# Kernel tuning notes

Measured on AMD Instinct MI355X. Metric: run time of the kernel, lower is better.

The kernel has to match this reference:

```python
import jax, jax.numpy as jnp
import numpy as np

D_MODEL, N_HEADS, D_HEAD, D_FF, N_LAYERS, VOCAB = 768, 12, 64, 3072, 4, 32000
B, S = 4, 1024
EPS = 1e-5
NEG = -1000000000.0


def layer_norm(x, gamma, beta):
    mean = jnp.mean(x, axis=-1, keepdims=True)
    var = jnp.mean((x - mean) ** 2, axis=-1, keepdims=True)
    return gamma * ((x - mean) / jnp.sqrt(var + EPS)) + beta


def gelu_lean(x):
    return x * (0.5 * (1.0 + jnp.tanh(0.7978845608 * (x + 0.044715 * x * x * x))))


def positional_encoding(seq_len, dim, dtype):
    idx = jnp.arange(dim)
    exponent = (2 * (idx // 2)).astype(dtype) / float(dim)
    pos = jnp.arange(seq_len, dtype=dtype)[:, None]
    angle = pos / jnp.power(jnp.asarray(10000.0, dtype), exponent[None, :])
    return jnp.where((idx % 2 == 0)[None, :], jnp.sin(angle), jnp.cos(angle))


def setup_inputs() -> dict:
    key = jax.random.key(0)
    ks = jax.random.split(key, 10)
    std = 0.02
    inp = {
        "tokens": jax.random.randint(ks[0], (B, S), 0, VOCAB),
        "predict_idx": 1023,
        "embedding": std * jax.random.normal(ks[1], (D_MODEL, VOCAB), jnp.float32),
        "ln1_g": jnp.ones((N_LAYERS, D_MODEL), jnp.float32),
        "ln1_b": jnp.zeros((N_LAYERS, D_MODEL), jnp.float32),
        "wq": std * jax.random.normal(ks[2], (N_LAYERS, N_HEADS, D_HEAD, D_MODEL), jnp.float32),
        "wk": std * jax.random.normal(ks[3], (N_LAYERS, N_HEADS, D_HEAD, D_MODEL), jnp.float32),
        "wv": std * jax.random.normal(ks[4], (N_LAYERS, N_HEADS, D_HEAD, D_MODEL), jnp.float32),
        "wo": std * jax.random.normal(ks[5], (N_LAYERS, D_MODEL, N_HEADS * D_HEAD), jnp.float32),
        "ln2_g": jnp.ones((N_LAYERS, D_MODEL), jnp.float32),
        "ln2_b": jnp.zeros((N_LAYERS, D_MODEL), jnp.float32),
        "fc1": std * jax.random.normal(ks[6], (N_LAYERS, D_FF, D_MODEL), jnp.float32),
        "fc2": std * jax.random.normal(ks[7], (N_LAYERS, D_MODEL, D_FF), jnp.float32),
        "lnf_g": jnp.ones((D_MODEL,), jnp.float32),
        "lnf_b": jnp.zeros((D_MODEL,), jnp.float32),
        "unembed": std * jax.random.normal(ks[8], (VOCAB, D_MODEL), jnp.float32),
    }
    return inp


def reference(tokens, predict_idx, embedding, ln1_g, ln1_b, wq, wk, wv, wo,
              ln2_g, ln2_b, fc1, fc2, lnf_g, lnf_b, unembed):
    dtype = embedding.dtype
    b, s = tokens.shape
    d_head = wq.shape[2]
    scale = 1.0 / float(np.sqrt(d_head))

    # token embedding [B,S,D] + sinusoidal positions
    x = embedding.T[tokens] + positional_encoding(s, embedding.shape[0], dtype)[None]

    # causal mask: True above the diagonal -> filled with -1e9
    causal = jnp.triu(jnp.ones((s, s), bool), k=1)

    for l in range(wq.shape[0]):
        h = layer_norm(x, ln1_g[l], ln1_b[l])
        q = jnp.einsum('bsd,hed->bhse', h, wq[l])
        k = jnp.einsum('bsd,hed->bhse', h, wk[l])
        v = jnp.einsum('bsd,hed->bhse', h, wv[l])
        scores = jnp.einsum('bhse,bhte->bhst', q, k) * scale
        scores = jnp.where(causal[None, None], NEG, scores)
        weights = jax.nn.softmax(scores, axis=-1)
        attn = jnp.einsum('bhst,bhte->bhse', weights, v)  # [B,H,S,dh]
        attn = attn.transpose(0, 2, 1, 3).reshape(b, s, -1)  # concat heads
        x = x + attn @ wo[l].T
        h2 = layer_norm(x, ln2_g[l], ln2_b[l])
        x = x + gelu_lean(h2 @ fc1[l].T) @ fc2[l].T

    selected = x[:, predict_idx, :]  # [B, D]
    normed = layer_norm(selected, lnf_g, lnf_b)
    return normed @ unembed.T  # [B, vocab]
```

## Files before the change

kernel.cpp:

```cpp
#include <hip/hip_runtime.h>
#include <hip/hip_bf16.h>

#define D_MODEL 768
#define N_HEADS 12
#define D_HEAD  64
#define D_FF    3072
#define N_LAYERS 4
#define VOCAB   32000
#define BATCH   4
#define SEQ     1024
#define NROWS   (BATCH*SEQ)
#define NEGV    -1000000000.0f
#define LN_EPS  1e-5f

typedef __attribute__((ext_vector_type(8))) short bf16x8;
typedef __attribute__((ext_vector_type(4))) float f32x4;
typedef __attribute__((ext_vector_type(8))) unsigned short u16x8;
typedef __attribute__((ext_vector_type(4))) unsigned short u16x4;

typedef __attribute__((address_space(1))) const unsigned int g_u32;
typedef __attribute__((address_space(3))) unsigned int l_u32;

__device__ __forceinline__ float bf2f(unsigned short u) {
  return __uint_as_float(((unsigned int)u) << 16);
}
__device__ __forceinline__ unsigned short f2bf(float f) {
  __hip_bfloat16 h = __float2bfloat16(f);
  return *reinterpret_cast<unsigned short*>(&h);
}

__device__ __forceinline__ float block_reduce_sum(float v, float* sbuf) {
#pragma unroll
  for (int off = 32; off > 0; off >>= 1) v += __shfl_down(v, off, 64);
  int lane = threadIdx.x & 63, wid = threadIdx.x >> 6;
  if (lane == 0) sbuf[wid] = v;
  __syncthreads();
  if (threadIdx.x == 0) sbuf[4] = sbuf[0] + sbuf[1] + sbuf[2] + sbuf[3];
  __syncthreads();
  return sbuf[4];
}

__device__ __forceinline__ float gelu_f(float x) {
  float z2 = 1.5957691216f * x * (1.0f + 0.044715f * x * x);
  return x / (1.0f + __expf(-z2));
}

__global__ __launch_bounds__(256) void qkv_pack_kernel(
    const float* __restrict__ wq, const float* __restrict__ wk,
    const float* __restrict__ wv, __hip_bfloat16* __restrict__ dst)
{
  const int WMAT = D_MODEL * D_MODEL;
  long long i = (long long)(blockIdx.x * 256 + threadIdx.x) * 8;
  long long l = i / (3LL * WMAT);
  long long rem = i - l * 3LL * WMAT;
  int which = (int)(rem / WMAT);
  long long off = rem - (long long)which * WMAT;
  const float* src = (which == 0 ? wq : which == 1 ? wk : wv) + l * WMAT + off;
  float4 a = *(const float4*)src;
  float4 b = *(const float4*)(src + 4);
  struct bf8 { __hip_bfloat16 h[8]; } r;
  r.h[0] = __float2bfloat16(a.x); r.h[1] = __float2bfloat16(a.y);
  r.h[2] = __float2bfloat16(a.z); r.h[3] = __float2bfloat16(a.w);
  r.h[4] = __float2bfloat16(b.x); r.h[5] = __float2bfloat16(b.y);
  r.h[6] = __float2bfloat16(b.z); r.h[7] = __float2bfloat16(b.w);
  *(bf8*)(dst + i) = r;
}

__global__ __launch_bounds__(256) void convert3_kernel(
    const float* __restrict__ wo, const float* __restrict__ fc1,
    const float* __restrict__ fc2, __hip_bfloat16* __restrict__ dst)
{
  const long long WM4 = 4LL * D_MODEL * D_MODEL;
  const long long FM4 = 4LL * D_FF * D_MODEL;
  long long i = (long long)(blockIdx.x * 256 + threadIdx.x) * 8;
  const float* src;
  if (i < WM4)            src = wo  + i;
  else if (i < WM4 + FM4) src = fc1 + (i - WM4);
  else                    src = fc2 + (i - WM4 - FM4);
  float4 a = *(const float4*)src;
  float4 b = *(const float4*)(src + 4);
  struct bf8 { __hip_bfloat16 h[8]; } r;
  r.h[0] = __float2bfloat16(a.x); r.h[1] = __float2bfloat16(a.y);
  r.h[2] = __float2bfloat16(a.z); r.h[3] = __float2bfloat16(a.w);
  r.h[4] = __float2bfloat16(b.x); r.h[5] = __float2bfloat16(b.y);
  r.h[6] = __float2bfloat16(b.z); r.h[7] = __float2bfloat16(b.w);
  *(bf8*)(dst + i) = r;
}

__global__ __launch_bounds__(256) void transpose_emb_kernel(
    const float* __restrict__ emb, __hip_bfloat16* __restrict__ embT)
{
  __shared__ float tile[64][65];
  const int vb = blockIdx.x * 64;
  const int db = blockIdx.y * 64;
  const int tid = threadIdx.x;
  {
    int r = tid >> 4, c = (tid & 15) * 4;
#pragma unroll
    for (int p = 0; p < 4; ++p) {
      float4 v = *(const float4*)(emb + (size_t)(db + r + p * 16) * VOCAB + vb + c);
      tile[c + 0][r + p * 16] = v.x;
      tile[c + 1][r + p * 16] = v.y;
      tile[c + 2][r + p * 16] = v.z;
      tile[c + 3][r + p * 16] = v.w;
    }
  }
  __syncthreads();
  {
    int v = tid >> 2, d0 = (tid & 3) * 16;
    unsigned short* op = (unsigned short*)embT + (size_t)(vb + v) * D_MODEL + db + d0;
    u16x8 o0, o1;
#pragma unroll
    for (int j = 0; j < 8; ++j) {
      o0[j] = f2bf(tile[v][d0 + j]);
      o1[j] = f2bf(tile[v][d0 + 8 + j]);
    }
    *(u16x8*)op = o0;
    *(u16x8*)(op + 8) = o1;
  }
}

__global__ __launch_bounds__(256) void embed_kernel(
    const int* __restrict__ tokens, const __hip_bfloat16* __restrict__ embT,
    float* __restrict__ x)
{
  int bs = blockIdx.x;
  int s = bs & (SEQ - 1);
  int tok = tokens[bs];
  const unsigned short* ep = (const unsigned short*)embT + (size_t)tok * D_MODEL;
  for (int d = threadIdx.x; d < D_MODEL; d += 256) {
    float ev = bf2f(ep[d]);
    int dpair = d & ~1;
    float expo = (float)dpair * (1.0f / (float)D_MODEL);
    float ang = (float)s / powf(10000.0f, expo);
    float pe = (d & 1) ? cosf(ang) : sinf(ang);
    x[(size_t)bs * D_MODEL + d] = ev + pe;
  }
}

__global__ __launch_bounds__(256) void ln_kernel(
    const float* __restrict__ in, __hip_bfloat16* __restrict__ out,
    const float* __restrict__ g, const float* __restrict__ bb)
{
  __shared__ float sbuf[8];
  size_t row = blockIdx.x;
  const float* rp = in + row * D_MODEL;
  int t = threadIdx.x;
  float x0 = rp[t], x1 = rp[t + 256], x2 = rp[t + 512];
  float mean = block_reduce_sum(x0 + x1 + x2, sbuf) * (1.0f / (float)D_MODEL);
  float d0 = x0 - mean, d1 = x1 - mean, d2 = x2 - mean;
  float var = block_reduce_sum(d0*d0 + d1*d1 + d2*d2, sbuf) * (1.0f / (float)D_MODEL);
  float rstd = rsqrtf(var + LN_EPS);
  __hip_bfloat16* op = out + row * D_MODEL;
  op[t]       = __float2bfloat16(g[t]       * (d0 * rstd) + bb[t]);
  op[t + 256] = __float2bfloat16(g[t + 256] * (d1 * rstd) + bb[t + 256]);
  op[t + 512] = __float2bfloat16(g[t + 512] * (d2 * rstd) + bb[t + 512]);
}

__global__ __launch_bounds__(256) void final_ln_kernel(
    const float* __restrict__ x, const int* __restrict__ pidx,
    const float* __restrict__ g, const float* __restrict__ bb,
    float* __restrict__ out)
{
  __shared__ float sbuf[8];
  int p = pidx[0];
  const float* rp = x + ((size_t)blockIdx.x * SEQ + p) * D_MODEL;
  int t = threadIdx.x;
  float x0 = rp[t], x1 = rp[t + 256], x2 = rp[t + 512];
  float mean = block_reduce_sum(x0 + x1 + x2, sbuf) * (1.0f / (float)D_MODEL);
  float d0 = x0 - mean, d1 = x1 - mean, d2 = x2 - mean;
  float var = block_reduce_sum(d0*d0 + d1*d1 + d2*d2, sbuf) * (1.0f / (float)D_MODEL);
  float rstd = rsqrtf(var + LN_EPS);
  float* op = out + (size_t)blockIdx.x * D_MODEL;
  op[t]       = g[t]       * (d0 * rstd) + bb[t];
  op[t + 256] = g[t + 256] * (d1 * rstd) + bb[t + 256];
  op[t + 512] = g[t + 512] * (d2 * rstd) + bb[t + 512];
}

__device__ __forceinline__ int2 xcd_tile(int gx, int gy) {
  int flat = blockIdx.y * gx + blockIdx.x;
  int cpx = (gx * gy) >> 3;
  int logical = (flat & 7) * cpx + (flat >> 3);
  return make_int2(logical % gx, logical / gx);
}

#define WAITV4() asm volatile("s_waitcnt vmcnt(4)" ::: "memory")
#define WAITV0() asm volatile("s_waitcnt vmcnt(0)" ::: "memory")
#define MEMFENCE() asm volatile("" ::: "memory")

__global__ __launch_bounds__(256) void gemm_bf16_kernel(
    const __hip_bfloat16* __restrict__ A, const __hip_bfloat16* __restrict__ W,
    void* __restrict__ Cv, const float* __restrict__ resid,
    int N, int K, int mode)
{
  __shared__ __align__(16) unsigned short As[3][128 * 32];
  __shared__ __align__(16) unsigned short Bs[3][128 * 32];
  const unsigned short* Au = (const unsigned short*)A;
  const unsigned short* Wu = (const unsigned short*)W;
  const int tid = threadIdx.x;
  const int wv = tid >> 6, ln = tid & 63;
  const int l15 = ln & 15, l4 = ln >> 4;
  int2 tc = xcd_tile(N >> 7, gridDim.y);
  const int bm = tc.y * 128, bn = tc.x * 128;
  const int wr = wv >> 1, wc = wv & 1;

  const int lrow = wv * 16 + (ln >> 2);
  const int schunk = (ln & 3) ^ ((ln >> 3) & 3);
  const size_t gA0 = (size_t)(bm + lrow) * K + schunk * 8;
  const size_t gA1 = (size_t)(bm + 64 + lrow) * K + schunk * 8;
  const size_t gB0 = (size_t)(bn + lrow) * K + schunk * 8;
  const size_t gB1 = (size_t)(bn + 64 + lrow) * K + schunk * 8;
  const int ldsb = wv * 512;

#define STAGE128(buf, k0)                                                          \
  {                                                                                \
    __builtin_amdgcn_global_load_lds((g_u32*)(Au + gA0 + (k0)), (l_u32*)(As[buf] + ldsb), 16, 0, 0);        \
    __builtin_amdgcn_global_load_lds((g_u32*)(Au + gA1 + (k0)), (l_u32*)(As[buf] + 2048 + ldsb), 16, 0, 0); \
    __builtin_amdgcn_global_load_lds((g_u32*)(Wu + gB0 + (k0)), (l_u32*)(Bs[buf] + ldsb), 16, 0, 0);        \
    __builtin_amdgcn_global_load_lds((g_u32*)(Wu + gB1 + (k0)), (l_u32*)(Bs[buf] + 2048 + ldsb), 16, 0, 0); \
  }

  const int rslot = (l4 ^ ((l15 >> 1) & 3)) * 8;

#define COMPUTE128(buf)                                                            \
  {                                                                                \
    bf16x8 af[4], bfr[4];                                                          \
    _Pragma("unroll")                                                              \
    for (int m = 0; m < 4; ++m)                                                    \
      af[m] = *(const bf16x8*)(As[buf] + (wr * 64 + m * 16 + l15) * 32 + rslot);   \
    _Pragma("unroll")                                                              \
    for (int n = 0; n < 4; ++n)                                                    \
      bfr[n] = *(const bf16x8*)(Bs[buf] + (wc * 64 + n * 16 + l15) * 32 + rslot);  \
    __builtin_amdgcn_s_setprio(1);                                                 \
    _Pragma("unroll")                                                              \
    for (int m = 0; m < 4; ++m)                                                    \
      _Pragma("unroll")                                                            \
      for (int n = 0; n < 4; ++n)                                                  \
        acc[m][n] = __builtin_amdgcn_mfma_f32_16x16x32_bf16(af[m], bfr[n], acc[m][n], 0, 0, 0); \
    __builtin_amdgcn_s_setprio(0);                                                 \
  }

  f32x4 acc[4][4];
#pragma unroll
  for (int m = 0; m < 4; ++m)
#pragma unroll
    for (int n = 0; n < 4; ++n) acc[m][n] = (f32x4){0.f, 0.f, 0.f, 0.f};

  const int NT = K >> 5;
  STAGE128(0, 0);
  STAGE128(1, 32);
  int cur = 0;
  for (int t = 0; t < NT - 1; ++t) {
    WAITV4();
    __builtin_amdgcn_s_barrier();
    MEMFENCE();
    if (t + 2 < NT) {
      int nxt = cur + 2; if (nxt >= 3) nxt -= 3;
      STAGE128(nxt, (t + 2) << 5);
    }
    COMPUTE128(cur);
    cur = (cur == 2) ? 0 : cur + 1;
  }
  WAITV0();
  __builtin_amdgcn_s_barrier();
  MEMFENCE();
  COMPUTE128(cur);

  float* Cf = (float*)Cv;
  __hip_bfloat16* Cb = (__hip_bfloat16*)Cv;
#pragma unroll
  for (int m = 0; m < 4; ++m) {
#pragma unroll
    for (int n = 0; n < 4; ++n) {
#pragma unroll
      for (int r = 0; r < 4; ++r) {
        int row = bm + wr * 64 + m * 16 + l4 * 4 + r;
        int col = bn + wc * 64 + n * 16 + l15;
        size_t off = (size_t)row * N + col;
        float v = acc[m][n][r];
        if (mode == 0)      Cf[off] = v;
        else if (mode == 1) Cf[off] = v + resid[off];
        else if (mode == 2) Cb[off] = __float2bfloat16(v);
        else                Cb[off] = __float2bfloat16(gelu_f(v));
      }
    }
  }
#undef STAGE128
#undef COMPUTE128
}

__global__ __launch_bounds__(256) void gemm64_bf16_kernel(
    const __hip_bfloat16* __restrict__ A, const __hip_bfloat16* __restrict__ W,
    void* __restrict__ Cv, const float* __restrict__ resid,
    int N, int K, int mode)
{
  __shared__ __align__(16) unsigned short As[3][64 * 64];
  __shared__ __align__(16) unsigned short Bs[3][64 * 64];
  const unsigned short* Au = (const unsigned short*)A;
  const unsigned short* Wu = (const unsigned short*)W;
  const int tid = threadIdx.x;
  const int wv = tid >> 6, ln = tid & 63;
  const int l15 = ln & 15, l4 = ln >> 4;
  int2 tc = xcd_tile(N >> 6, gridDim.y);
  const int bm = tc.y * 64, bn = tc.x * 64;
  const int wr = wv >> 1, wc = wv & 1;

  const int srow = tid >> 3;
  const int schunk = (tid & 7) ^ ((tid >> 3) & 7);
  const size_t gA0 = (size_t)(bm + srow) * K + schunk * 8;
  const size_t gA1 = (size_t)(bm + 32 + srow) * K + schunk * 8;
  const size_t gB0 = (size_t)(bn + srow) * K + schunk * 8;
  const size_t gB1 = (size_t)(bn + 32 + srow) * K + schunk * 8;
  const int ldsb = wv * 512;

#define STAGE64(buf, k0)                                                           \
  {                                                                                \
    __builtin_amdgcn_global_load_lds((g_u32*)(Au + gA0 + (k0)), (l_u32*)(As[buf] + ldsb), 16, 0, 0);        \
    __builtin_amdgcn_global_load_lds((g_u32*)(Au + gA1 + (k0)), (l_u32*)(As[buf] + 2048 + ldsb), 16, 0, 0); \
    __builtin_amdgcn_global_load_lds((g_u32*)(Wu + gB0 + (k0)), (l_u32*)(Bs[buf] + ldsb), 16, 0, 0);        \
    __builtin_amdgcn_global_load_lds((g_u32*)(Wu + gB1 + (k0)), (l_u32*)(Bs[buf] + 2048 + ldsb), 16, 0, 0); \
  }

#define COMPUTE64(buf)                                                             \
  {                                                                                \
    bf16x8 af[2][2], bfr[2][2];                                                    \
    _Pragma("unroll")                                                              \
    for (int ks = 0; ks < 2; ++ks) {                                               \
      _Pragma("unroll")                                                            \
      for (int m = 0; m < 2; ++m)                                                  \
        af[ks][m] = *(const bf16x8*)(As[buf] + (wr * 32 + m * 16 + l15) * 64 +     \
                                     (((ks * 4 + l4) ^ (l15 & 7)) << 3));          \
      _Pragma("unroll")                                                            \
      for (int n = 0; n < 2; ++n)                                                  \
        bfr[ks][n] = *(const bf16x8*)(Bs[buf] + (wc * 32 + n * 16 + l15) * 64 +    \
                                      (((ks * 4 + l4) ^ (l15 & 7)) << 3));         \
    }                                                                              \
    __builtin_amdgcn_s_setprio(1);                                                 \
    _Pragma("unroll")                                                              \
    for (int ks = 0; ks < 2; ++ks)                                                 \
      _Pragma("unroll")                                                            \
      for (int m = 0; m < 2; ++m)                                                  \
        _Pragma("unroll")                                                          \
        for (int n = 0; n < 2; ++n)                                                \
          acc[m][n] = __builtin_amdgcn_mfma_f32_16x16x32_bf16(af[ks][m], bfr[ks][n], acc[m][n], 0, 0, 0); \
    __builtin_amdgcn_s_setprio(0);                                                 \
  }

  f32x4 acc[2][2];
#pragma unroll
  for (int m = 0; m < 2; ++m)
#pragma unroll
    for (int n = 0; n < 2; ++n) acc[m][n] = (f32x4){0.f, 0.f, 0.f, 0.f};

  const int NT = K >> 6;
  STAGE64(0, 0);
  STAGE64(1, 64);
  int cur = 0;
  for (int t = 0; t < NT - 1; ++t) {
    WAITV4();
    __builtin_amdgcn_s_barrier();
    MEMFENCE();
    if (t + 2 < NT) {
      int nxt = cur + 2; if (nxt >= 3) nxt -= 3;
      STAGE64(nxt, (t + 2) << 6);
    }
    COMPUTE64(cur);
    cur = (cur == 2) ? 0 : cur + 1;
  }
  WAITV0();
  __builtin_amdgcn_s_barrier();
  MEMFENCE();
  COMPUTE64(cur);

  float* Cf = (float*)Cv;
  __hip_bfloat16* Cb = (__hip_bfloat16*)Cv;
#pragma unroll
  for (int m = 0; m < 2; ++m) {
#pragma unroll
    for (int n = 0; n < 2; ++n) {
#pragma unroll
      for (int r = 0; r < 4; ++r) {
        int row = bm + wr * 32 + m * 16 + l4 * 4 + r;
        int col = bn + wc * 32 + n * 16 + l15;
        size_t off = (size_t)row * N + col;
        float v = acc[m][n][r];
        if (mode == 0)      Cf[off] = v;
        else if (mode == 1) Cf[off] = v + resid[off];
        else if (mode == 2) Cb[off] = __float2bfloat16(v);
        else                Cb[off] = __float2bfloat16(gelu_f(v));
      }
    }
  }
#undef STAGE64
#undef COMPUTE64
}

__global__ __launch_bounds__(128) void flash_attn_kernel(
    const __hip_bfloat16* __restrict__ qkv_, __hip_bfloat16* __restrict__ attn_)
{
  const unsigned short* qkv = (const unsigned short*)qkv_;
  unsigned short* attn = (unsigned short*)attn_;
  const int px = blockIdx.x;
  const int h  = blockIdx.y;
  const int b  = blockIdx.z;
  const int tid = threadIdx.x;
  const int wq = tid >> 6, ln = tid & 63;
  const int l15 = ln & 15, l4 = ln >> 4;

  __shared__ unsigned short Ks[2][64 * 64];
  __shared__ unsigned short Vt[2][64 * 64];
  __shared__ unsigned short Pw[2][16 * 64];

  const int krow = tid >> 3;
  const int kchunk = (tid & 7) ^ ((tid >> 3) & 7);
  const int kldsbase = (tid & 64) * 8;

  const int vc = tid & 7;
  const int vp = tid >> 3;
  const int vtr = (2 * vp) & 7;
  const int vtb0 = vp >> 2;

  u16x8 v0, v1, v2, v3;

#define STAGE_K(buf, t0)                                                           \
  {                                                                                \
    _Pragma("unroll")                                                              \
    for (int j = 0; j < 4; ++j) {                                                  \
      const unsigned short* gk = qkv +                                             \
          (size_t)(b * SEQ + (t0) + j * 16 + krow) * 2304 + 768 + h * 64 + kchunk * 8; \
      __builtin_amdgcn_global_load_lds((g_u32*)gk,                                 \
          (l_u32*)(Ks[buf] + j * 1024 + kldsbase), 16, 0, 0);                      \
    }                                                                              \
  }

#define LOAD_V(t0)                                                                 \
  {                                                                                \
    const unsigned short* gv = qkv +                                               \
        (size_t)(b * SEQ + (t0) + 2 * vp) * 2304 + 1536 + h * 64 + vc * 8;         \
    v0 = *(const u16x8*)gv;                                                        \
    v1 = *(const u16x8*)(gv + 2304);                                               \
    v2 = *(const u16x8*)(gv + 32 * 2304);                                          \
    v3 = *(const u16x8*)(gv + 33 * 2304);                                          \
  }

#define WRITE_VT(buf)                                                              \
  {                                                                                \
    _Pragma("unroll")                                                              \
    for (int j = 0; j < 8; ++j) {                                                  \
      int e = vc * 8 + j;                                                          \
      unsigned int w01 = (unsigned int)(unsigned short)v0[j] |                     \
                         ((unsigned int)(unsigned short)v1[j] << 16);              \
      unsigned int w23 = (unsigned int)(unsigned short)v2[j] |                     \
                         ((unsigned int)(unsigned short)v3[j] << 16);              \
      *(unsigned int*)(Vt[buf] + e * 64 + ((vtb0 ^ (e & 7)) << 3) + vtr) = w01;    \
      *(unsigned int*)(Vt[buf] + e * 64 + (((vtb0 + 4) ^ (e & 7)) << 3) + vtr) = w23; \
    }                                                                              \
  }

  for (int pass = 0; pass < 2; ++pass) {
    const int qi = (pass == 0) ? px : 31 - px;
    const int s0 = qi * 32;
    const int ntiles = (qi >> 1) + 1;
    const int qg = s0 + wq * 16 + l15;

    bf16x8 qf[2];
    {
      const size_t qbase = (size_t)(b * SEQ + qg) * 2304 + h * 64;
#pragma unroll
      for (int ks = 0; ks < 2; ++ks) {
        u16x8 raw = *(const u16x8*)(qkv + qbase + ks * 32 + l4 * 8);
        bf16x8 q;
#pragma unroll
        for (int j = 0; j < 8; ++j) q[j] = (short)f2bf(bf2f(raw[j]) * 0.125f);
        qf[ks] = q;
      }
    }

    float mrow = -1e30f, lrow = 0.f;
    f32x4 o[4];
#pragma unroll
    for (int n = 0; n < 4; ++n) o[n] = (f32x4){0.f, 0.f, 0.f, 0.f};

    STAGE_K(0, 0);
    LOAD_V(0);
    WAITV0();
    WRITE_VT(0);
    __syncthreads();

    for (int t = 0; t < ntiles; ++t) {
      const int cur = t & 1;
      const bool pfn = (t + 1 < ntiles);
      if (pfn) { STAGE_K(cur ^ 1, (t + 1) * 64); LOAD_V((t + 1) * 64); }

      f32x4 sf[4];
#pragma unroll
      for (int n = 0; n < 4; ++n) sf[n] = (f32x4){0.f, 0.f, 0.f, 0.f};
      __builtin_amdgcn_s_setprio(1);
#pragma unroll
      for (int ks = 0; ks < 2; ++ks) {
#pragma unroll
        for (int n = 0; n < 4; ++n) {
          int tr = n * 16 + l15;
          bf16x8 kf = *(const bf16x8*)(Ks[cur] + tr * 64 + (((ks * 4 + l4) ^ (tr & 7)) << 3));
          sf[n] = __builtin_amdgcn_mfma_f32_16x16x32_bf16(kf, qf[ks], sf[n], 0, 0, 0);
        }
      }
      __builtin_amdgcn_s_setprio(0);

      if (t == ntiles - 1) {
#pragma unroll
        for (int n = 0; n < 4; ++n) {
#pragma unroll
          for (int r = 0; r < 4; ++r) {
            int tg = t * 64 + n * 16 + l4 * 4 + r;
            if (tg > qg) sf[n][r] = NEGV;
          }
        }
      }

      float mx = sf[0][0];
#pragma unroll
      for (int n = 0; n < 4; ++n)
#pragma unroll
        for (int r = 0; r < 4; ++r) mx = fmaxf(mx, sf[n][r]);
      mx = fmaxf(mx, __shfl_xor(mx, 16));
      mx = fmaxf(mx, __shfl_xor(mx, 32));
      float mnew = fmaxf(mrow, mx);
      float alpha = __expf(mrow - mnew);
      float pb[4][4];
      float sum = 0.f;
#pragma unroll
      for (int n = 0; n < 4; ++n)
#pragma unroll
        for (int r = 0; r < 4; ++r) {
          float p = __expf(sf[n][r] - mnew);
          pb[n][r] = p;
          sum += p;
        }
      sum += __shfl_xor(sum, 16);
      sum += __shfl_xor(sum, 32);
      lrow = lrow * alpha + sum;
      mrow = mnew;

      float ar[4];
#pragma unroll
      for (int r = 0; r < 4; ++r)
        ar[r] = __shfl(alpha, (ln & 48) | (l4 * 4 + r));
#pragma unroll
      for (int n = 0; n < 4; ++n)
#pragma unroll
        for (int r = 0; r < 4; ++r) o[n][r] *= ar[r];

      unsigned short* Pme = Pw[wq];
#pragma unroll
      for (int n = 0; n < 4; ++n) {
        int tb = 2 * n + (l4 >> 1);
        u16x4 w;
        w[0] = f2bf(pb[n][0]); w[1] = f2bf(pb[n][1]);
        w[2] = f2bf(pb[n][2]); w[3] = f2bf(pb[n][3]);
        *(u16x4*)(Pme + l15 * 64 + ((tb ^ (l15 & 7)) << 3) + (l4 & 1) * 4) = w;
      }

      __builtin_amdgcn_s_setprio(1);
#pragma unroll
      for (int ks = 0; ks < 2; ++ks) {
        bf16x8 pf = *(const bf16x8*)(Pme + l15 * 64 + (((ks * 4 + l4) ^ (l15 & 7)) << 3));
#pragma unroll
        for (int n = 0; n < 4; ++n) {
          int e = n * 16 + l15;
          bf16x8 vf = *(const bf16x8*)(Vt[cur] + e * 64 + (((ks * 4 + l4) ^ (e & 7)) << 3));
          o[n] = __builtin_amdgcn_mfma_f32_16x16x32_bf16(pf, vf, o[n], 0, 0, 0);
        }
      }
      __builtin_amdgcn_s_setprio(0);

      if (pfn) { WAITV0(); WRITE_VT(cur ^ 1); }
      __syncthreads();
    }

    float lr[4];
#pragma unroll
    for (int r = 0; r < 4; ++r)
      lr[r] = __shfl(lrow, (ln & 48) | (l4 * 4 + r));
#pragma unroll
    for (int r = 0; r < 4; ++r) {
      float inv = 1.0f / lr[r];
      size_t base = (size_t)(b * SEQ + s0 + wq * 16 + l4 * 4 + r) * D_MODEL + h * 64;
#pragma unroll
      for (int n = 0; n < 4; ++n)
        attn[base + n * 16 + l15] = f2bf(o[n][r] * inv);
    }
  }
#undef STAGE_K
#undef LOAD_V
#undef WRITE_VT
}

__global__ __launch_bounds__(256) void logits_kernel(
    const float* __restrict__ normed, const float* __restrict__ unemb,
    float* __restrict__ out)
{
  __shared__ __align__(16) float ns[BATCH][D_MODEL];
  for (int d = threadIdx.x; d < BATCH * D_MODEL; d += 256)
    ((float*)ns)[d] = normed[d];
  __syncthreads();
  int g = threadIdx.x >> 4, li = threadIdx.x & 15;
  int v = blockIdx.x * 16 + g;
  const float* up = unemb + (size_t)v * D_MODEL;
  float s0 = 0.f, s1 = 0.f, s2 = 0.f, s3 = 0.f;
#pragma unroll
  for (int it = 0; it < D_MODEL / 64; ++it) {
    int e = it * 64 + li * 4;
    float4 u = *(const float4*)(up + e);
    float4 n0 = *(const float4*)&ns[0][e];
    float4 n1 = *(const float4*)&ns[1][e];
    float4 n2 = *(const float4*)&ns[2][e];
    float4 n3 = *(const float4*)&ns[3][e];
    s0 += u.x*n0.x + u.y*n0.y + u.z*n0.z + u.w*n0.w;
    s1 += u.x*n1.x + u.y*n1.y + u.z*n1.z + u.w*n1.w;
    s2 += u.x*n2.x + u.y*n2.y + u.z*n2.z + u.w*n2.w;
    s3 += u.x*n3.x + u.y*n3.y + u.z*n3.z + u.w*n3.w;
  }
#pragma unroll
  for (int msk = 1; msk < 16; msk <<= 1) {
    s0 += __shfl_xor(s0, msk, 64); s1 += __shfl_xor(s1, msk, 64);
    s2 += __shfl_xor(s2, msk, 64); s3 += __shfl_xor(s3, msk, 64);
  }
  if (li == 0) {
    out[(size_t)0 * VOCAB + v] = s0;
    out[(size_t)1 * VOCAB + v] = s1;
    out[(size_t)2 * VOCAB + v] = s2;
    out[(size_t)3 * VOCAB + v] = s3;
  }
}

extern "C" void kernel_launch(void* const* d_in, const int* in_sizes, int n_in,
                              void* d_out, int out_size, void* d_ws, size_t ws_size,
                              hipStream_t stream) {
  const int*   tokens = (const int*)d_in[0];
  const int*   pidx   = (const int*)d_in[1];
  const float* emb    = (const float*)d_in[2];
  const float* ln1_g  = (const float*)d_in[3];
  const float* ln1_b  = (const float*)d_in[4];
  const float* wq     = (const float*)d_in[5];
  const float* wk     = (const float*)d_in[6];
  const float* wv     = (const float*)d_in[7];
  const float* wo     = (const float*)d_in[8];
  const float* ln2_g  = (const float*)d_in[9];
  const float* ln2_b  = (const float*)d_in[10];
  const float* fc1    = (const float*)d_in[11];
  const float* fc2    = (const float*)d_in[12];
  const float* lnf_g  = (const float*)d_in[13];
  const float* lnf_b  = (const float*)d_in[14];
  const float* unemb  = (const float*)d_in[15];
  float* out = (float*)d_out;

  char* wp = (char*)d_ws;
  const size_t NX = (size_t)NROWS * D_MODEL;
  float* x = (float*)wp;                  wp += NX * 4;
  float* normed = (float*)wp;             wp += BATCH * D_MODEL * 4;
  __hip_bfloat16* h    = (__hip_bfloat16*)wp; wp += NX * 2;
  __hip_bfloat16* attn = (__hip_bfloat16*)wp; wp += NX * 2;
  __hip_bfloat16* qkvb = (__hip_bfloat16*)wp; wp += (size_t)NROWS * 2304 * 2;
  __hip_bfloat16* ffn  = (__hip_bfloat16*)wp; wp += (size_t)NROWS * D_FF * 2;
  __hip_bfloat16* wqkvb = (__hip_bfloat16*)wp; wp += (size_t)N_LAYERS * 2304 * D_MODEL * 2;
  __hip_bfloat16* wob   = (__hip_bfloat16*)wp; wp += (size_t)N_LAYERS * D_MODEL * D_MODEL * 2;
  __hip_bfloat16* fc1b  = (__hip_bfloat16*)wp; wp += (size_t)N_LAYERS * D_FF * D_MODEL * 2;
  __hip_bfloat16* fc2b  = (__hip_bfloat16*)wp; wp += (size_t)N_LAYERS * D_MODEL * D_FF * 2;

  __hip_bfloat16* embT = attn;

  const int WMAT = D_MODEL * D_MODEL;
  const int FMAT = D_FF * D_MODEL;

  transpose_emb_kernel<<<dim3(VOCAB / 64, D_MODEL / 64), 256, 0, stream>>>(emb, embT);
  embed_kernel<<<NROWS, 256, 0, stream>>>(tokens, embT, x);

  qkv_pack_kernel<<<N_LAYERS * 3 * WMAT / 2048, 256, 0, stream>>>(wq, wk, wv, wqkvb);
  convert3_kernel<<<(N_LAYERS * (WMAT + 2 * FMAT)) / 2048, 256, 0, stream>>>(wo, fc1, fc2, wob);

  for (int l = 0; l < N_LAYERS; ++l) {
    const size_t qofs = (size_t)l * 3 * WMAT;
    const size_t wofs = (size_t)l * WMAT;
    const size_t fofs = (size_t)l * FMAT;

    ln_kernel<<<NROWS, 256, 0, stream>>>(x, h, ln1_g + l * D_MODEL, ln1_b + l * D_MODEL);

    gemm_bf16_kernel<<<dim3(2304 / 128, NROWS / 128), 256, 0, stream>>>(
        h, wqkvb + qofs, qkvb, nullptr, 2304, D_MODEL, 2);

    flash_attn_kernel<<<dim3(16, N_HEADS, BATCH), 128, 0, stream>>>(qkvb, attn);

    gemm64_bf16_kernel<<<dim3(D_MODEL / 64, NROWS / 64), 256, 0, stream>>>(
        attn, wob + wofs, x, x, D_MODEL, D_MODEL, 1);

    ln_kernel<<<NROWS, 256, 0, stream>>>(x, h, ln2_g + l * D_MODEL, ln2_b + l * D_MODEL);

    gemm_bf16_kernel<<<dim3(D_FF / 128, NROWS / 128), 256, 0, stream>>>(
        h, fc1b + fofs, ffn, nullptr, D_FF, D_MODEL, 3);

    gemm64_bf16_kernel<<<dim3(D_MODEL / 64, NROWS / 64), 256, 0, stream>>>(
        ffn, fc2b + fofs, x, x, D_MODEL, D_FF, 1);
  }

  final_ln_kernel<<<BATCH, 256, 0, stream>>>(x, pidx, lnf_g, lnf_b, normed);
  logits_kernel<<<VOCAB / 16, 256, 0, stream>>>(normed, unemb, out);
}
```

Measured before the change: 785.7 us.

## Split-K the FFN down-projection GEMM with separate fp32 reduction kernel

Replaces the fc2 GEMM (K=3072) with a two-way split-K variant that uses a triple-buffered LDS pipeline and writes fp32 partial tiles into the reused attn/qkv workspace. A new reduce kernel then adds both partials into the residual stream x. The aim is more blocks in flight and shorter per-block K loops for better CU occupancy. The cost is an extra kernel launch plus writing and re-reading about 25 MB of fp32 partials per layer.

```diff
diff --git a/kernel.cpp b/kernel.cpp
--- a/kernel.cpp
+++ b/kernel.cpp
@@ -395,6 +395,117 @@
 #undef COMPUTE64
 }
 
+__global__ __launch_bounds__(256) void gemm64sk_bf16_kernel(
+    const __hip_bfloat16* __restrict__ A, const __hip_bfloat16* __restrict__ W,
+    float* __restrict__ part, int N, int Ksub, int lda)
+{
+  __shared__ __align__(16) unsigned short As[3][64 * 64];
+  __shared__ __align__(16) unsigned short Bs[3][64 * 64];
+  const unsigned short* Au = (const unsigned short*)A;
+  const unsigned short* Wu = (const unsigned short*)W;
+  const int tid = threadIdx.x;
+  const int wv = tid >> 6, ln = tid & 63;
+  const int l15 = ln & 15, l4 = ln >> 4;
+  int2 tc = xcd_tile(N >> 6, gridDim.y);
+  const int bm = tc.y * 64, bn = tc.x * 64;
+  const int wr = wv >> 1, wc = wv & 1;
+  const int kz = blockIdx.z * Ksub;
+
+  const int srow = tid >> 3;
+  const int schunk = (tid & 7) ^ ((tid >> 3) & 7);
+  const size_t gA0 = (size_t)(bm + srow) * lda + kz + schunk * 8;
+  const size_t gA1 = (size_t)(bm + 32 + srow) * lda + kz + schunk * 8;
+  const size_t gB0 = (size_t)(bn + srow) * lda + kz + schunk * 8;
+  const size_t gB1 = (size_t)(bn + 32 + srow) * lda + kz + schunk * 8;
+  const int ldsb = wv * 512;
+
+#define STAGESK(buf, k0)                                                           \
+  {                                                                                \
+    __builtin_amdgcn_global_load_lds((g_u32*)(Au + gA0 + (k0)), (l_u32*)(As[buf] + ldsb), 16, 0, 0);        \
+    __builtin_amdgcn_global_load_lds((g_u32*)(Au + gA1 + (k0)), (l_u32*)(As[buf] + 2048 + ldsb), 16, 0, 0); \
+    __builtin_amdgcn_global_load_lds((g_u32*)(Wu + gB0 + (k0)), (l_u32*)(Bs[buf] + ldsb), 16, 0, 0);        \
+    __builtin_amdgcn_global_load_lds((g_u32*)(Wu + gB1 + (k0)), (l_u32*)(Bs[buf] + 2048 + ldsb), 16, 0, 0); \
+  }
+
+#define COMPUTESK(buf)                                                             \
+  {                                                                                \
+    bf16x8 af[2][2], bfr[2][2];                                                    \
+    _Pragma("unroll")                                                              \
+    for (int ks = 0; ks < 2; ++ks) {                                               \
+      _Pragma("unroll")                                                            \
+      for (int m = 0; m < 2; ++m)                                                  \
+        af[ks][m] = *(const bf16x8*)(As[buf] + (wr * 32 + m * 16 + l15) * 64 +     \
+                                     (((ks * 4 + l4) ^ (l15 & 7)) << 3));          \
+      _Pragma("unroll")                                                            \
+      for (int n = 0; n < 2; ++n)                                                  \
+        bfr[ks][n] = *(const bf16x8*)(Bs[buf] + (wc * 32 + n * 16 + l15) * 64 +    \
+                                      (((ks * 4 + l4) ^ (l15 & 7)) << 3));         \
+    }                                                                              \
+    __builtin_amdgcn_s_setprio(1);                                                 \
+    _Pragma("unroll")                                                              \
+    for (int ks = 0; ks < 2; ++ks)                                                 \
+      _Pragma("unroll")                                                            \
+      for (int m = 0; m < 2; ++m)                                                  \
+        _Pragma("unroll")                                                          \
+        for (int n = 0; n < 2; ++n)                                                \
+          acc[m][n] = __builtin_amdgcn_mfma_f32_16x16x32_bf16(af[ks][m], bfr[ks][n], acc[m][n], 0, 0, 0); \
+    __builtin_amdgcn_s_setprio(0);                                                 \
+  }
+
+  f32x4 acc[2][2];
+#pragma unroll
+  for (int m = 0; m < 2; ++m)
+#pragma unroll
+    for (int n = 0; n < 2; ++n) acc[m][n] = (f32x4){0.f, 0.f, 0.f, 0.f};
+
+  const int NT = Ksub >> 6;
+  STAGESK(0, 0);
+  STAGESK(1, 64);
+  int cur = 0;
+  for (int t = 0; t < NT - 1; ++t) {
+    WAITV4();
+    __builtin_amdgcn_s_barrier();
+    MEMFENCE();
+    if (t + 2 < NT) {
+      int nxt = cur + 2; if (nxt >= 3) nxt -= 3;
+      STAGESK(nxt, (t + 2) << 6);
+    }
+    COMPUTESK(cur);
+    cur = (cur == 2) ? 0 : cur + 1;
+  }
+  WAITV0();
+  __builtin_amdgcn_s_barrier();
+  MEMFENCE();
+  COMPUTESK(cur);
+
+  float* out = part + (size_t)blockIdx.z * ((size_t)gridDim.y * 64) * N;
+#pragma unroll
+  for (int m = 0; m < 2; ++m) {
+#pragma unroll
+    for (int n = 0; n < 2; ++n) {
+#pragma unroll
+      for (int r = 0; r < 4; ++r) {
+        int row = bm + wr * 32 + m * 16 + l4 * 4 + r;
+        int col = bn + wc * 32 + n * 16 + l15;
+        out[(size_t)row * N + col] = acc[m][n][r];
+      }
+    }
+  }
+#undef STAGESK
+#undef COMPUTESK
+}
+
+__global__ __launch_bounds__(256) void reduce2_kernel(
+    float* __restrict__ x, const float* __restrict__ part, size_t n)
+{
+  size_t i = ((size_t)blockIdx.x * 256 + threadIdx.x) * 4;
+  float4 a = *(float4*)(x + i);
+  float4 b = *(const float4*)(part + i);
+  float4 c = *(const float4*)(part + n + i);
+  a.x += b.x + c.x; a.y += b.y + c.y; a.z += b.z + c.z; a.w += b.w + c.w;
+  *(float4*)(x + i) = a;
+}
+
 __global__ __launch_bounds__(128) void flash_attn_kernel(
     const __hip_bfloat16* __restrict__ qkv_, __hip_bfloat16* __restrict__ attn_)
 {
@@ -669,6 +780,7 @@
   __hip_bfloat16* fc2b  = (__hip_bfloat16*)wp; wp += (size_t)N_LAYERS * D_MODEL * D_FF * 2;
 
   __hip_bfloat16* embT = attn;
+  float* skpart = (float*)attn;
 
   const int WMAT = D_MODEL * D_MODEL;
   const int FMAT = D_FF * D_MODEL;
@@ -699,8 +811,9 @@
     gemm_bf16_kernel<<<dim3(D_FF / 128, NROWS / 128), 256, 0, stream>>>(
         h, fc1b + fofs, ffn, nullptr, D_FF, D_MODEL, 3);
 
-    gemm64_bf16_kernel<<<dim3(D_MODEL / 64, NROWS / 64), 256, 0, stream>>>(
-        ffn, fc2b + fofs, x, x, D_MODEL, D_FF, 1);
+    gemm64sk_bf16_kernel<<<dim3(D_MODEL / 64, NROWS / 64, 2), 256, 0, stream>>>(
+        ffn, fc2b + fofs, skpart, D_MODEL, D_FF / 2, D_FF);
+    reduce2_kernel<<<(int)(NX / 1024), 256, 0, stream>>>(x, skpart, NX);
   }
 
   final_ln_kernel<<<BATCH, 256, 0, stream>>>(x, pidx, lnf_g, lnf_b, normed);
```

New measurement: 802.2 us. +2.1%, slower.
